# Kernel optimization log

Hardware: AMD Instinct MI355X
Metric: run time of the kernel (lower is better)

## Reference

```python
import jax, jax.numpy as jnp
import numpy as np

N_NODES = 50000
N_EDGES = 800000
EPS = 1e-12  # F.normalize default eps


def spmm(edge_row, edge_col, edge_val, dense):
    # sparse [N,N] (COO edges) @ dense [N,D] -> [N,D]
    gathered = edge_val[:, None] * dense[edge_col]          # [E, D]
    return jax.ops.segment_sum(gathered, edge_row, num_segments=N_NODES)


def setup_inputs() -> dict:
    key = jax.random.key(0)
    ks = jax.random.split(key, 8)
    x = jax.random.normal(ks[0], (N_NODES, 300), dtype=jnp.float32)
    edge_row = jax.random.randint(ks[1], (N_EDGES,), 0, N_NODES, dtype=jnp.int32)
    edge_col = jax.random.randint(ks[2], (N_EDGES,), 0, N_NODES, dtype=jnp.int32)
    edge_val = jax.random.uniform(ks[3], (N_EDGES,), dtype=jnp.float32)
    W1 = jax.random.normal(ks[4], (256, 300), dtype=jnp.float32) * 0.05
    b1 = jax.random.normal(ks[5], (256,), dtype=jnp.float32) * 0.05
    W2 = jax.random.normal(ks[6], (128, 256), dtype=jnp.float32) * 0.05
    b2 = jax.random.normal(ks[7], (128,), dtype=jnp.float32) * 0.05
    return {"x": x, "edge_row": edge_row, "edge_col": edge_col,
            "edge_val": edge_val, "W1": W1, "b1": b1, "W2": W2, "b2": b2}


def reference(x, edge_row, edge_col, edge_val, W1, b1, W2, b2):
    # GraphConv 1: X @ W1.T, SpMM with adj, +bias, ReLU (dropout is eval no-op)
    h = x @ W1.T                                            # [N, 256]
    h = spmm(edge_row, edge_col, edge_val, h) + b1
    h = jax.nn.relu(h)
    # GraphConv last: no ReLU
    h = h @ W2.T                                            # [N, 128]
    h = spmm(edge_row, edge_col, edge_val, h) + b2
    # F.normalize(x): row-wise L2 normalize with eps clamp
    norm = jnp.linalg.norm(h, axis=1, keepdims=True)
    return h / jnp.maximum(norm, EPS)
```

## Files before the change

kernel.cpp:

```cpp
#include <hip/hip_runtime.h>
#include <math.h>

#define NN 50000
#define NE 800000
#define ESLICE 200192

typedef __bf16 bf16x8 __attribute__((ext_vector_type(8)));
typedef __bf16 bf16x4 __attribute__((ext_vector_type(4)));
typedef float f32x4 __attribute__((ext_vector_type(4)));

__device__ __forceinline__ void gload16(const void* g, void* l){
  __builtin_amdgcn_global_load_lds((const __attribute__((address_space(1))) void*)g,
                                   (__attribute__((address_space(3))) void*)l, 16, 0, 0);
}


__global__ void k_zero_i32(int* __restrict__ p, int n){
  int i = blockIdx.x * blockDim.x + threadIdx.x;
  if (i < n) p[i] = 0;
}

__global__ __launch_bounds__(256)
void k_rank(const int* __restrict__ erow, int* __restrict__ cnt, int* __restrict__ pos){
  const int t = blockIdx.x * 256 + threadIdx.x;
  #pragma unroll
  for (int k = 0; k < 4; ++k){
    const int e = t + k * ESLICE;
    if (e < NE){
      const int r = erow[e];
      pos[e] = atomicAdd(&cnt[r], 1);
    }
  }
}

__global__ __launch_bounds__(256)
void k_scan1(const int* __restrict__ cnt, int* __restrict__ rs, int* __restrict__ part, int n){
  const int t = threadIdx.x, b = blockIdx.x;
  const int i = b * 256 + t;
  int v = (i < n) ? cnt[i] : 0;
  const int lane = t & 63, w = t >> 6;
  int s = v;
  #pragma unroll
  for (int d = 1; d < 64; d <<= 1){ int u = __shfl_up(s, d); if (lane >= d) s += u; }
  __shared__ int wsum[4];
  if (lane == 63) wsum[w] = s;
  __syncthreads();
  int add = 0;
  #pragma unroll
  for (int k = 0; k < 4; ++k) if (k < w) add += wsum[k];
  s += add;
  if (i < n) rs[i + 1] = s;
  if (t == 255) part[b] = s;
}

__global__ __launch_bounds__(256)
void k_scan2(int* __restrict__ part, int nb){
  const int t = threadIdx.x;
  int v = (t < nb) ? part[t] : 0;
  const int lane = t & 63, w = t >> 6;
  int s = v;
  #pragma unroll
  for (int d = 1; d < 64; d <<= 1){ int u = __shfl_up(s, d); if (lane >= d) s += u; }
  __shared__ int wsum[4];
  if (lane == 63) wsum[w] = s;
  __syncthreads();
  int add = 0;
  #pragma unroll
  for (int k = 0; k < 4; ++k) if (k < w) add += wsum[k];
  s += add;
  if (t < nb) part[t] = s - v;
}

__global__ __launch_bounds__(256)
void k_scan3(int* __restrict__ rs, const int* __restrict__ part, int n){
  const int i = blockIdx.x * 256 + threadIdx.x;
  if (i < n) rs[i + 1] += part[blockIdx.x];
  if (i == 0) rs[0] = 0;
}

__global__ __launch_bounds__(256)
void k_scatter2(const int* __restrict__ erow, const int* __restrict__ ecol,
                const float* __restrict__ evalv, const int* __restrict__ rs,
                const int* __restrict__ pos, int2* __restrict__ out){
  const int t = blockIdx.x * 256 + threadIdx.x;
  #pragma unroll
  for (int k = 0; k < 4; ++k){
    const int e = t + k * ESLICE;
    if (e < NE){
      const int r = erow[e];
      const int p = rs[r] + pos[e];
      out[p] = make_int2(ecol[e], __float_as_int(evalv[e]));
    }
  }
}


__global__ __launch_bounds__(256)
void conv_bf16(const float* __restrict__ src, __bf16* __restrict__ dst,
               int M, int K, int Kp){
  const int q = blockIdx.x * 256 + threadIdx.x;
  const int perRow = Kp >> 2;
  const int r = q / perRow;
  const int k = (q - r * perRow) << 2;
  float4 v = make_float4(0.f, 0.f, 0.f, 0.f);
  if (r < M && k < K) v = *(const float4*)(src + (size_t)r * K + k);
  bf16x4 o;
  o[0] = (__bf16)v.x; o[1] = (__bf16)v.y; o[2] = (__bf16)v.z; o[3] = (__bf16)v.w;
  *(bf16x4*)(dst + (size_t)r * Kp + k) = o;
}

__global__ void k_zero_bf16(__bf16* __restrict__ p, int n4){
  int i = blockIdx.x * blockDim.x + threadIdx.x;
  if (i < n4){ bf16x4 z = {}; *(bf16x4*)(p + (size_t)i * 4) = z; }
}


template<int KT>
__global__ __launch_bounds__(256)
void gemm_bf16(const __bf16* __restrict__ A, const __bf16* __restrict__ B,
               __bf16* __restrict__ C, int ld, int N){
  __shared__ char ldsbuf[49152];
  const int tid = threadIdx.x;
  const int lane = tid & 63;
  const int bn = blockIdx.x * 64;
  const int bm = blockIdx.y * 128;
  const int wr = (tid >> 7) & 1;
  const int wc = (tid >> 6) & 1;

  f32x4 acc[4][2];
  #pragma unroll
  for (int i = 0; i < 4; ++i)
    #pragma unroll
    for (int j = 0; j < 2; ++j) acc[i][j] = (f32x4){0.f, 0.f, 0.f, 0.f};

  auto stage = [&](int kt, int sel){
    char* lb = ldsbuf + sel * 24576;
    #pragma unroll
    for (int i = 0; i < 4; ++i){
      const int d = i * 4096 + tid * 16;
      const int row = d >> 7;
      const int colb = (d & 127) ^ ((row & 7) << 4);
      const __bf16* gp = A + (size_t)(bm + row) * ld + kt * 64 + (colb >> 1);
      gload16(gp, lb + i * 4096 + (tid & 192) * 16);
    }
    #pragma unroll
    for (int i = 0; i < 2; ++i){
      const int d = i * 4096 + tid * 16;
      const int row = d >> 7;
      const int colb = (d & 127) ^ ((row & 7) << 4);
      const __bf16* gp = B + (size_t)(bn + row) * ld + kt * 64 + (colb >> 1);
      gload16(gp, lb + 16384 + i * 4096 + (tid & 192) * 16);
    }
  };

  auto compute = [&](int sel){
    const char* lA = ldsbuf + sel * 24576;
    const char* lB = lA + 16384;
    #pragma unroll
    for (int c = 0; c < 2; ++c){
      bf16x8 av[4], bv[2];
      #pragma unroll
      for (int i = 0; i < 4; ++i){
        const int row = wr * 64 + i * 16 + (lane & 15);
        const int colb = (c * 64 + ((lane >> 4) << 4)) ^ ((row & 7) << 4);
        av[i] = *(const bf16x8*)(lA + row * 128 + colb);
      }
      #pragma unroll
      for (int j = 0; j < 2; ++j){
        const int row = wc * 32 + j * 16 + (lane & 15);
        const int colb = (c * 64 + ((lane >> 4) << 4)) ^ ((row & 7) << 4);
        bv[j] = *(const bf16x8*)(lB + row * 128 + colb);
      }
      #pragma unroll
      for (int i = 0; i < 4; ++i)
        #pragma unroll
        for (int j = 0; j < 2; ++j)
          acc[i][j] = __builtin_amdgcn_mfma_f32_16x16x32_bf16(av[i], bv[j], acc[i][j], 0, 0, 0);
    }
  };

  stage(0, 0);
  for (int kt = 0; kt < KT; ++kt){
    __syncthreads();
    if (kt + 1 < KT) stage(kt + 1, (kt + 1) & 1);
    compute(kt & 1);
  }

  __syncthreads();
  float* lw = (float*)ldsbuf;
  #pragma unroll
  for (int i = 0; i < 4; ++i)
    #pragma unroll
    for (int j = 0; j < 2; ++j)
      #pragma unroll
      for (int r = 0; r < 4; ++r){
        const int row = wr * 64 + i * 16 + ((lane >> 4) << 2) + r;
        const int col = wc * 32 + j * 16 + (lane & 15);
        lw[row * 68 + col] = acc[i][j][r];
      }
  __syncthreads();
  #pragma unroll
  for (int p = 0; p < 4; ++p){
    const int row = p * 32 + (tid >> 3);
    const int col8 = (tid & 7) * 8;
    const float4 v0 = *(const float4*)&lw[row * 68 + col8];
    const float4 v1 = *(const float4*)&lw[row * 68 + col8 + 4];
    bf16x8 o;
    o[0] = (__bf16)v0.x; o[1] = (__bf16)v0.y; o[2] = (__bf16)v0.z; o[3] = (__bf16)v0.w;
    o[4] = (__bf16)v1.x; o[5] = (__bf16)v1.y; o[6] = (__bf16)v1.z; o[7] = (__bf16)v1.w;
    *(bf16x8*)(C + (size_t)(bm + row) * N + bn + col8) = o;
  }
}


__global__ __launch_bounds__(256)
void spmm_bias_relu_b16(const int2* __restrict__ ecv, const int* __restrict__ start,
                        const __bf16* __restrict__ H, const float* __restrict__ bias,
                        __bf16* __restrict__ out){
  const int w = (blockIdx.x * 256 + threadIdx.x) >> 6;
  const int lane = threadIdx.x & 63;
  const int half = lane >> 5, sl = lane & 31;
  if (w >= NN) return;
  const int s = start[w], e = start[w + 1];
  float a[8];
  #pragma unroll
  for (int k = 0; k < 8; ++k) a[k] = 0.f;
  for (int base = s; base < e; base += 64){
    int2 cv = make_int2(0, 0);
    if (base + lane < e) cv = ecv[base + lane];
    const int m = min(64, e - base);
    for (int j2 = 0; 4 * j2 < m; ++j2){
      const int idx0 = 4 * j2 + half;
      const int idx1 = idx0 + 2;
      int c0 = __shfl(cv.x, idx0);
      float v0 = __int_as_float(__shfl(cv.y, idx0));
      int c1 = __shfl(cv.x, idx1);
      float v1 = __int_as_float(__shfl(cv.y, idx1));
      if (idx0 >= m){ c0 = 0; v0 = 0.f; }
      if (idx1 >= m){ c1 = 0; v1 = 0.f; }
      const bf16x8 h0 = *(const bf16x8*)(H + (size_t)c0 * 256 + sl * 8);
      const bf16x8 h1 = *(const bf16x8*)(H + (size_t)c1 * 256 + sl * 8);
      #pragma unroll
      for (int k = 0; k < 8; ++k) a[k] = fmaf(v0, (float)h0[k], a[k]);
      #pragma unroll
      for (int k = 0; k < 8; ++k) a[k] = fmaf(v1, (float)h1[k], a[k]);
    }
  }
  #pragma unroll
  for (int k = 0; k < 8; ++k) a[k] += __shfl_xor(a[k], 32);
  const float4 b0 = *(const float4*)(bias + sl * 8);
  const float4 b1 = *(const float4*)(bias + sl * 8 + 4);
  bf16x8 o;
  o[0] = (__bf16)fmaxf(a[0] + b0.x, 0.f);
  o[1] = (__bf16)fmaxf(a[1] + b0.y, 0.f);
  o[2] = (__bf16)fmaxf(a[2] + b0.z, 0.f);
  o[3] = (__bf16)fmaxf(a[3] + b0.w, 0.f);
  o[4] = (__bf16)fmaxf(a[4] + b1.x, 0.f);
  o[5] = (__bf16)fmaxf(a[5] + b1.y, 0.f);
  o[6] = (__bf16)fmaxf(a[6] + b1.z, 0.f);
  o[7] = (__bf16)fmaxf(a[7] + b1.w, 0.f);
  if (half == 0) *(bf16x8*)(out + (size_t)w * 256 + sl * 8) = o;
}

__global__ __launch_bounds__(256)
void spmm_bias_norm_b16(const int2* __restrict__ ecv, const int* __restrict__ start,
                        const __bf16* __restrict__ H, const float* __restrict__ bias,
                        float* __restrict__ out){
  const int w = (blockIdx.x * 256 + threadIdx.x) >> 6;
  const int lane = threadIdx.x & 63;
  const int quar = lane >> 4, sl = lane & 15;
  if (w >= NN) return;
  const int s = start[w], e = start[w + 1];
  float a[8];
  #pragma unroll
  for (int k = 0; k < 8; ++k) a[k] = 0.f;
  for (int base = s; base < e; base += 64){
    int2 cv = make_int2(0, 0);
    if (base + lane < e) cv = ecv[base + lane];
    const int m = min(64, e - base);
    for (int j2 = 0; 8 * j2 < m; ++j2){
      const int idx0 = 8 * j2 + quar;
      const int idx1 = idx0 + 4;
      int c0 = __shfl(cv.x, idx0);
      float v0 = __int_as_float(__shfl(cv.y, idx0));
      int c1 = __shfl(cv.x, idx1);
      float v1 = __int_as_float(__shfl(cv.y, idx1));
      if (idx0 >= m){ c0 = 0; v0 = 0.f; }
      if (idx1 >= m){ c1 = 0; v1 = 0.f; }
      const bf16x8 h0 = *(const bf16x8*)(H + (size_t)c0 * 128 + sl * 8);
      const bf16x8 h1 = *(const bf16x8*)(H + (size_t)c1 * 128 + sl * 8);
      #pragma unroll
      for (int k = 0; k < 8; ++k) a[k] = fmaf(v0, (float)h0[k], a[k]);
      #pragma unroll
      for (int k = 0; k < 8; ++k) a[k] = fmaf(v1, (float)h1[k], a[k]);
    }
  }
  #pragma unroll
  for (int k = 0; k < 8; ++k){
    a[k] += __shfl_xor(a[k], 32);
    a[k] += __shfl_xor(a[k], 16);
  }
  const float4 b0 = *(const float4*)(bias + sl * 8);
  const float4 b1 = *(const float4*)(bias + sl * 8 + 4);
  float f[8];
  f[0] = a[0] + b0.x; f[1] = a[1] + b0.y; f[2] = a[2] + b0.z; f[3] = a[3] + b0.w;
  f[4] = a[4] + b1.x; f[5] = a[5] + b1.y; f[6] = a[6] + b1.z; f[7] = a[7] + b1.w;
  float ss = 0.f;
  #pragma unroll
  for (int k = 0; k < 8; ++k) ss = fmaf(f[k], f[k], ss);
  #pragma unroll
  for (int m2 = 1; m2 < 16; m2 <<= 1) ss += __shfl_xor(ss, m2);
  const float inv = 1.f / fmaxf(sqrtf(ss), 1e-12f);
  if (quar == 0){
    float4 o0 = make_float4(f[0] * inv, f[1] * inv, f[2] * inv, f[3] * inv);
    float4 o1 = make_float4(f[4] * inv, f[5] * inv, f[6] * inv, f[7] * inv);
    *(float4*)(out + (size_t)w * 128 + sl * 8) = o0;
    *(float4*)(out + (size_t)w * 128 + sl * 8 + 4) = o1;
  }
}


extern "C" void kernel_launch(void* const* d_in, const int* in_sizes, int n_in,
                              void* d_out, int out_size, void* d_ws, size_t ws_size,
                              hipStream_t stream){
  const float* x    = (const float*)d_in[0];
  const int*   erow = (const int*)d_in[1];
  const int*   ecol = (const int*)d_in[2];
  const float* evalv= (const float*)d_in[3];
  const float* W1   = (const float*)d_in[4];
  const float* b1   = (const float*)d_in[5];
  const float* W2   = (const float*)d_in[6];
  const float* b2   = (const float*)d_in[7];
  float* out = (float*)d_out;

  char* ws = (char*)d_ws;
  __bf16* xb  = (__bf16*)(ws);
  __bf16* W1b = (__bf16*)(ws + 32030720);
  __bf16* W2b = (__bf16*)(ws + 32194560);
  __bf16* h1  = (__bf16*)(ws + 32260096);
  __bf16* h2  = (__bf16*)(ws + 57884672);
  __bf16* h3  = (__bf16*)(ws + 83509248);
  int2*   ecv = (int2*)(ws + 96321536);
  int*    rs  = (int*)(ws + 102721536);
  int*    part= (int*)(ws + 102921552);
  int*    cur = (int*)(ws + 102922368);
  int*    pos = (int*)(ws + 32260096);

  k_zero_i32<<<196, 256, 0, stream>>>(cur, NN);
  k_rank<<<782, 256, 0, stream>>>(erow, cur, pos);
  k_scan1<<<196, 256, 0, stream>>>(cur, rs, part, NN);
  k_scan2<<<1, 256, 0, stream>>>(part, 196);
  k_scan3<<<196, 256, 0, stream>>>(rs, part, NN);
  k_scatter2<<<782, 256, 0, stream>>>(erow, ecol, evalv, rs, pos, ecv);

  conv_bf16<<<15640, 256, 0, stream>>>(x, xb, NN, 300, 320);
  conv_bf16<<<80, 256, 0, stream>>>(W1, W1b, 256, 300, 320);
  conv_bf16<<<32, 256, 0, stream>>>(W2, W2b, 128, 256, 256);

  gemm_bf16<5><<<dim3(4, 391), 256, 0, stream>>>(xb, W1b, h1, 320, 256);
  spmm_bias_relu_b16<<<12500, 256, 0, stream>>>(ecv, rs, h1, b1, h2);
  k_zero_bf16<<<12, 256, 0, stream>>>(h2 + (size_t)NN * 256, 3072);

  gemm_bf16<4><<<dim3(2, 391), 256, 0, stream>>>(h2, W2b, h3, 256, 128);
  spmm_bias_norm_b16<<<12500, 256, 0, stream>>>(ecv, rs, h3, b2, out);
}
```

Before: 210.8 us.

## Split first SpMM into channel halves, unroll gathers, swizzle GEMM tiles

```diff
diff --git a/kernel.cpp b/kernel.cpp
--- a/kernel.cpp
+++ b/kernel.cpp
@@ -3,7 +3,7 @@
 
 #define NN 50000
 #define NE 800000
-#define ESLICE 200192
+#define ESLICE 100096
 
 typedef __bf16 bf16x8 __attribute__((ext_vector_type(8)));
 typedef __bf16 bf16x4 __attribute__((ext_vector_type(4)));
@@ -24,7 +24,7 @@
 void k_rank(const int* __restrict__ erow, int* __restrict__ cnt, int* __restrict__ pos){
   const int t = blockIdx.x * 256 + threadIdx.x;
   #pragma unroll
-  for (int k = 0; k < 4; ++k){
+  for (int k = 0; k < 8; ++k){
     const int e = t + k * ESLICE;
     if (e < NE){
       const int r = erow[e];
@@ -84,7 +84,7 @@
                 const int* __restrict__ pos, int2* __restrict__ out){
   const int t = blockIdx.x * 256 + threadIdx.x;
   #pragma unroll
-  for (int k = 0; k < 4; ++k){
+  for (int k = 0; k < 8; ++k){
     const int e = t + k * ESLICE;
     if (e < NE){
       const int r = erow[e];
@@ -109,21 +109,36 @@
   *(bf16x4*)(dst + (size_t)r * Kp + k) = o;
 }
 
-__global__ void k_zero_bf16(__bf16* __restrict__ p, int n4){
-  int i = blockIdx.x * blockDim.x + threadIdx.x;
-  if (i < n4){ bf16x4 z = {}; *(bf16x4*)(p + (size_t)i * 4) = z; }
-}
-
-
-template<int KT>
+__global__ __launch_bounds__(256)
+void conv_w(const float* __restrict__ W1, const float* __restrict__ W2,
+            __bf16* __restrict__ W1b, __bf16* __restrict__ W2b){
+  const int b = blockIdx.x;
+  const float* src; __bf16* dst; int q, K, Kp;
+  if (b < 80){ src = W1; dst = W1b; q = b * 256 + threadIdx.x; K = 300; Kp = 320; }
+  else       { src = W2; dst = W2b; q = (b - 80) * 256 + threadIdx.x; K = 256; Kp = 256; }
+  const int perRow = Kp >> 2;
+  const int r = q / perRow;
+  const int k = (q - r * perRow) << 2;
+  float4 v = make_float4(0.f, 0.f, 0.f, 0.f);
+  if (k < K) v = *(const float4*)(src + (size_t)r * K + k);
+  bf16x4 o;
+  o[0] = (__bf16)v.x; o[1] = (__bf16)v.y; o[2] = (__bf16)v.z; o[3] = (__bf16)v.w;
+  *(bf16x4*)(dst + (size_t)r * Kp + k) = o;
+}
+
+
+template<int KT, int LGN>
 __global__ __launch_bounds__(256)
 void gemm_bf16(const __bf16* __restrict__ A, const __bf16* __restrict__ B,
                __bf16* __restrict__ C, int ld, int N){
   __shared__ char ldsbuf[49152];
   const int tid = threadIdx.x;
   const int lane = tid & 63;
-  const int bn = blockIdx.x * 64;
-  const int bm = blockIdx.y * 128;
+  const int L = blockIdx.x;
+  const int bmt = (L & 7) + ((L >> (3 + LGN)) << 3);
+  if (bmt >= 391) return;
+  const int bm = bmt * 128;
+  const int bn = ((L >> 3) & ((1 << LGN) - 1)) * 64;
   const int wr = (tid >> 7) & 1;
   const int wc = (tid >> 6) & 1;
 
@@ -214,12 +229,12 @@
 
 
 __global__ __launch_bounds__(256)
-void spmm_bias_relu_b16(const int2* __restrict__ ecv, const int* __restrict__ start,
-                        const __bf16* __restrict__ H, const float* __restrict__ bias,
-                        __bf16* __restrict__ out){
+void spmm_relu_half(const int2* __restrict__ ecv, const int* __restrict__ start,
+                    const __bf16* __restrict__ H, const float* __restrict__ bias,
+                    __bf16* __restrict__ out, int ch0){
   const int w = (blockIdx.x * 256 + threadIdx.x) >> 6;
   const int lane = threadIdx.x & 63;
-  const int half = lane >> 5, sl = lane & 31;
+  const int quar = lane >> 4, sl = lane & 15;
   if (w >= NN) return;
   const int s = start[w], e = start[w + 1];
   float a[8];
@@ -229,27 +244,32 @@
     int2 cv = make_int2(0, 0);
     if (base + lane < e) cv = ecv[base + lane];
     const int m = min(64, e - base);
-    for (int j2 = 0; 4 * j2 < m; ++j2){
-      const int idx0 = 4 * j2 + half;
-      const int idx1 = idx0 + 2;
-      int c0 = __shfl(cv.x, idx0);
-      float v0 = __int_as_float(__shfl(cv.y, idx0));
-      int c1 = __shfl(cv.x, idx1);
-      float v1 = __int_as_float(__shfl(cv.y, idx1));
-      if (idx0 >= m){ c0 = 0; v0 = 0.f; }
-      if (idx1 >= m){ c1 = 0; v1 = 0.f; }
-      const bf16x8 h0 = *(const bf16x8*)(H + (size_t)c0 * 256 + sl * 8);
-      const bf16x8 h1 = *(const bf16x8*)(H + (size_t)c1 * 256 + sl * 8);
-      #pragma unroll
-      for (int k = 0; k < 8; ++k) a[k] = fmaf(v0, (float)h0[k], a[k]);
-      #pragma unroll
-      for (int k = 0; k < 8; ++k) a[k] = fmaf(v1, (float)h1[k], a[k]);
-    }
-  }
-  #pragma unroll
-  for (int k = 0; k < 8; ++k) a[k] += __shfl_xor(a[k], 32);
-  const float4 b0 = *(const float4*)(bias + sl * 8);
-  const float4 b1 = *(const float4*)(bias + sl * 8 + 4);
+    for (int j2 = 0; 16 * j2 < m; ++j2){
+      int cc[4]; float vv[4];
+      #pragma unroll
+      for (int u = 0; u < 4; ++u){
+        const int idx = 16 * j2 + quar + 4 * u;
+        cc[u] = __shfl(cv.x, idx);
+        vv[u] = __int_as_float(__shfl(cv.y, idx));
+        if (idx >= m){ cc[u] = 0; vv[u] = 0.f; }
+      }
+      bf16x8 h[4];
+      #pragma unroll
+      for (int u = 0; u < 4; ++u)
+        h[u] = *(const bf16x8*)(H + (size_t)cc[u] * 256 + ch0 + sl * 8);
+      #pragma unroll
+      for (int u = 0; u < 4; ++u)
+        #pragma unroll
+        for (int k = 0; k < 8; ++k) a[k] = fmaf(vv[u], (float)h[u][k], a[k]);
+    }
+  }
+  #pragma unroll
+  for (int k = 0; k < 8; ++k){
+    a[k] += __shfl_xor(a[k], 32);
+    a[k] += __shfl_xor(a[k], 16);
+  }
+  const float4 b0 = *(const float4*)(bias + ch0 + sl * 8);
+  const float4 b1 = *(const float4*)(bias + ch0 + sl * 8 + 4);
   bf16x8 o;
   o[0] = (__bf16)fmaxf(a[0] + b0.x, 0.f);
   o[1] = (__bf16)fmaxf(a[1] + b0.y, 0.f);
@@ -259,7 +279,7 @@
   o[5] = (__bf16)fmaxf(a[5] + b1.y, 0.f);
   o[6] = (__bf16)fmaxf(a[6] + b1.z, 0.f);
   o[7] = (__bf16)fmaxf(a[7] + b1.w, 0.f);
-  if (half == 0) *(bf16x8*)(out + (size_t)w * 256 + sl * 8) = o;
+  if (quar == 0) *(bf16x8*)(out + (size_t)w * 256 + ch0 + sl * 8) = o;
 }
 
 __global__ __launch_bounds__(256)
@@ -278,21 +298,23 @@
     int2 cv = make_int2(0, 0);
     if (base + lane < e) cv = ecv[base + lane];
     const int m = min(64, e - base);
-    for (int j2 = 0; 8 * j2 < m; ++j2){
-      const int idx0 = 8 * j2 + quar;
-      const int idx1 = idx0 + 4;
-      int c0 = __shfl(cv.x, idx0);
-      float v0 = __int_as_float(__shfl(cv.y, idx0));
-      int c1 = __shfl(cv.x, idx1);
-      float v1 = __int_as_float(__shfl(cv.y, idx1));
-      if (idx0 >= m){ c0 = 0; v0 = 0.f; }
-      if (idx1 >= m){ c1 = 0; v1 = 0.f; }
-      const bf16x8 h0 = *(const bf16x8*)(H + (size_t)c0 * 128 + sl * 8);
-      const bf16x8 h1 = *(const bf16x8*)(H + (size_t)c1 * 128 + sl * 8);
-      #pragma unroll
-      for (int k = 0; k < 8; ++k) a[k] = fmaf(v0, (float)h0[k], a[k]);
-      #pragma unroll
-      for (int k = 0; k < 8; ++k) a[k] = fmaf(v1, (float)h1[k], a[k]);
+    for (int j2 = 0; 16 * j2 < m; ++j2){
+      int cc[4]; float vv[4];
+      #pragma unroll
+      for (int u = 0; u < 4; ++u){
+        const int idx = 16 * j2 + quar + 4 * u;
+        cc[u] = __shfl(cv.x, idx);
+        vv[u] = __int_as_float(__shfl(cv.y, idx));
+        if (idx >= m){ cc[u] = 0; vv[u] = 0.f; }
+      }
+      bf16x8 h[4];
+      #pragma unroll
+      for (int u = 0; u < 4; ++u)
+        h[u] = *(const bf16x8*)(H + (size_t)cc[u] * 128 + sl * 8);
+      #pragma unroll
+      for (int u = 0; u < 4; ++u)
+        #pragma unroll
+        for (int k = 0; k < 8; ++k) a[k] = fmaf(vv[u], (float)h[u][k], a[k]);
     }
   }
   #pragma unroll
@@ -347,20 +369,19 @@
   int*    pos = (int*)(ws + 32260096);
 
   k_zero_i32<<<196, 256, 0, stream>>>(cur, NN);
-  k_rank<<<782, 256, 0, stream>>>(erow, cur, pos);
+  k_rank<<<391, 256, 0, stream>>>(erow, cur, pos);
   k_scan1<<<196, 256, 0, stream>>>(cur, rs, part, NN);
   k_scan2<<<1, 256, 0, stream>>>(part, 196);
   k_scan3<<<196, 256, 0, stream>>>(rs, part, NN);
-  k_scatter2<<<782, 256, 0, stream>>>(erow, ecol, evalv, rs, pos, ecv);
+  k_scatter2<<<391, 256, 0, stream>>>(erow, ecol, evalv, rs, pos, ecv);
 
   conv_bf16<<<15640, 256, 0, stream>>>(x, xb, NN, 300, 320);
-  conv_bf16<<<80, 256, 0, stream>>>(W1, W1b, 256, 300, 320);
-  conv_bf16<<<32, 256, 0, stream>>>(W2, W2b, 128, 256, 256);
-
-  gemm_bf16<5><<<dim3(4, 391), 256, 0, stream>>>(xb, W1b, h1, 320, 256);
-  spmm_bias_relu_b16<<<12500, 256, 0, stream>>>(ecv, rs, h1, b1, h2);
-  k_zero_bf16<<<12, 256, 0, stream>>>(h2 + (size_t)NN * 256, 3072);
-
-  gemm_bf16<4><<<dim3(2, 391), 256, 0, stream>>>(h2, W2b, h3, 256, 128);
+  conv_w<<<112, 256, 0, stream>>>(W1, W2, W1b, W2b);
+
+  gemm_bf16<5, 2><<<1568, 256, 0, stream>>>(xb, W1b, h1, 320, 256);
+  spmm_relu_half<<<12500, 256, 0, stream>>>(ecv, rs, h1, b1, h2, 0);
+  spmm_relu_half<<<12500, 256, 0, stream>>>(ecv, rs, h1, b1, h2, 128);
+
+  gemm_bf16<4, 1><<<784, 256, 0, stream>>>(h2, W2b, h3, 256, 128);
   spmm_bias_norm_b16<<<12500, 256, 0, stream>>>(ecv, rs, h3, b2, out);
 }
```

Measured after the change: 197.4 us. -6.4%, faster.
